# Kernel optimization log

Hardware: AMD Instinct MI355X
Metric: run time of the kernel (lower is better)

## Reference

```python
import jax, jax.numpy as jnp
import numpy as np

NUM_HEADS = 12


def setup_inputs() -> dict:
    key = jax.random.key(0)
    k1, k2, k3, k4 = jax.random.split(key, 4)
    dim = 768
    B, N1, N2 = 8, 64, 4096  # N1 must equal head_dim = dim // num_heads
    x = jax.random.normal(k1, (B, N1, dim), dtype=jnp.float32)
    y = jax.random.normal(k2, (B, N2, dim), dtype=jnp.float32)
    # torch nn.Linear layout: [out_features, in_features]
    W_qkv = jax.random.normal(k3, (3 * dim, dim), dtype=jnp.float32) * 0.02
    W_proj = jax.random.normal(k4, (dim, dim), dtype=jnp.float32) * 0.02
    b_proj = jnp.zeros((dim,), dtype=jnp.float32)
    return {"x": x, "y": y, "W_qkv": W_qkv, "W_proj": W_proj, "b_proj": b_proj}


def _split_heads(t, H):
    # [B, N, C] -> [B, H, N, C//H]
    B, N, C = t.shape
    return t.reshape(B, N, H, C // H).transpose(0, 2, 1, 3)


def reference(x, y, W_qkv, W_proj, b_proj):
    H = NUM_HEADS
    B1, N1, C = x.shape
    B2, N2, _ = y.shape
    hd = C // H
    scale = hd ** -0.5

    # qkv projections (bias=False); take q from x, k/v from y
    qkv_x = x @ W_qkv.T                      # [B, N1, 3C]
    q = _split_heads(qkv_x[..., :C], H)      # [B, H, N1, hd]
    qkv_y = y @ W_qkv.T                      # [B, N2, 3C]
    k = _split_heads(qkv_y[..., C:2 * C], H)  # [B, H, N2, hd]
    v = _split_heads(qkv_y[..., 2 * C:], H)   # [B, H, N2, hd]

    attn = jnp.einsum('bhqd,bhkd->bhqk', q, k) * scale  # [B, H, N1, N2]
    attn = jax.nn.softmax(attn, axis=-1)
    attn_t = attn.transpose(0, 1, 3, 2)       # [B, H, N2, N1]; N1 == hd

    # non-standard elementwise combine with v (requires N1 == hd)
    out = attn_t * v                          # [B, H, N2, hd]
    out = out.transpose(0, 2, 1, 3).reshape(B2, N2, C)
    return out @ W_proj.T + b_proj
```

## Files before the change

kernel.cpp:

```cpp
#include <hip/hip_runtime.h>
#include <math.h>


typedef __attribute__((ext_vector_type(8))) short short8;
typedef __attribute__((ext_vector_type(4))) float f32x4;

__device__ __forceinline__ ushort f2bf(float x) {
  unsigned u = __float_as_uint(x);
  u += 0x7fffu + ((u >> 16) & 1u);
  return (ushort)(u >> 16);
}
__device__ __forceinline__ float bf2f(ushort h) {
  return __uint_as_float((unsigned)h << 16);
}

__device__ __forceinline__ void gl_lds16(const ushort* g, ushort* l) {
  __builtin_amdgcn_global_load_lds(
      (__attribute__((address_space(1))) void*)g,
      (__attribute__((address_space(3))) void*)l, 16, 0, 0);
}

__global__ __launch_bounds__(256) void cast_all(
    const float* __restrict__ x, ushort* __restrict__ xb,
    const float* __restrict__ w1, ushort* __restrict__ w1b,
    const float* __restrict__ w2, ushort* __restrict__ w2b,
    const float* __restrict__ y, ushort* __restrict__ yb) {
  long i = (long)(blockIdx.x * 256 + threadIdx.x) * 8;
  if (i >= 27918336L) return;
  const float* s; ushort* d; long off;
  if (i < 393216L)        { s = x;  d = xb;  off = i; }
  else if (i < 2162688L)  { s = w1; d = w1b; off = i - 393216L; }
  else if (i < 2752512L)  { s = w2; d = w2b; off = i - 2162688L; }
  else                    { s = y;  d = yb;  off = i - 2752512L; }
  float4 a = *(const float4*)(s + off);
  float4 b = *(const float4*)(s + off + 4);
  ushort o[8] = {f2bf(a.x), f2bf(a.y), f2bf(a.z), f2bf(a.w),
                 f2bf(b.x), f2bf(b.y), f2bf(b.z), f2bf(b.w)};
  *(uint4*)(d + off) = *(const uint4*)o;
}

template <typename CT>
__device__ __forceinline__ void gemm_body(
    const ushort* __restrict__ A, int lda,
    const ushort* __restrict__ B, int ldb,
    CT* __restrict__ C, int ldc, int K,
    const float* __restrict__ bias, int rt, int ct)
{
  __shared__ __align__(16) ushort As[2][8192];
  __shared__ __align__(16) ushort Bs[2][4096];
  const int tid = threadIdx.x;
  const int m0 = rt * 256, n0 = ct * 128;

  const int w = tid >> 6, lane = tid & 63;
  const int lm = lane & 15, quad = lane >> 4;
  const int WR = (w >> 1) * 128, WC = (w & 1) * 64;

  const ushort* Ag[4];
#pragma unroll
  for (int q = 0; q < 4; ++q) {
    const int G = q * 256 + w * 64 + lane;
    const int row = G >> 2, g = ((G & 3) - (row >> 1)) & 3;
    Ag[q] = A + (size_t)(m0 + row) * lda + g * 8;
  }
  const ushort* Bg[2];
#pragma unroll
  for (int q = 0; q < 2; ++q) {
    const int G = q * 256 + w * 64 + lane;
    const int row = G >> 2, g = ((G & 3) - (row >> 1)) & 3;
    Bg[q] = B + (size_t)(n0 + row) * ldb + g * 8;
  }

  f32x4 acc[8][4];
#pragma unroll
  for (int i = 0; i < 8; ++i)
#pragma unroll
    for (int j = 0; j < 4; ++j) acc[i][j] = (f32x4)(0.f);

  const int nk = K >> 5;
#pragma unroll
  for (int q = 0; q < 4; ++q) gl_lds16(Ag[q], &As[0][q * 2048 + w * 512]);
#pragma unroll
  for (int q = 0; q < 2; ++q) gl_lds16(Bg[q], &Bs[0][q * 2048 + w * 512]);

  int cur = 0;
  for (int kk = 0; kk < nk; ++kk) {
    __syncthreads();
    if (kk + 1 < nk) {
      const int k0 = (kk + 1) << 5;
#pragma unroll
      for (int q = 0; q < 4; ++q) gl_lds16(Ag[q] + k0, &As[cur ^ 1][q * 2048 + w * 512]);
#pragma unroll
      for (int q = 0; q < 2; ++q) gl_lds16(Bg[q] + k0, &Bs[cur ^ 1][q * 2048 + w * 512]);
    }
    const ushort* Ab = &As[cur][0];
    const ushort* Bb = &Bs[cur][0];
    short8 af[8], bf8[4];
#pragma unroll
    for (int i = 0; i < 8; ++i) {
      const int Ra = WR + i * 16 + lm;
      af[i] = *(const short8*)(const void*)(Ab + Ra * 32 + ((quad + (Ra >> 1)) & 3) * 8);
    }
#pragma unroll
    for (int j = 0; j < 4; ++j) {
      const int Rb = WC + j * 16 + lm;
      bf8[j] = *(const short8*)(const void*)(Bb + Rb * 32 + ((quad + (Rb >> 1)) & 3) * 8);
    }
#pragma unroll
    for (int i = 0; i < 8; ++i)
#pragma unroll
      for (int j = 0; j < 4; ++j)
        acc[i][j] = __builtin_amdgcn_mfma_f32_16x16x32_bf16(af[i], bf8[j], acc[i][j], 0, 0, 0);
    cur ^= 1;
  }
  __syncthreads();

  if constexpr (sizeof(CT) == 2) {
    ushort* eb = ((ushort*)&As[0][0]) + w * 2048;
#pragma unroll
    for (int i = 0; i < 8; ++i) {
      ushort* ebc = eb + (i & 1) * 1024;
#pragma unroll
      for (int j = 0; j < 4; ++j)
#pragma unroll
        for (int r = 0; r < 4; ++r) {
          const int R = quad * 4 + r;
          const int gt = j * 2 + (lm >> 3);
          const int gs = (gt + R) & 7;
          ebc[R * 64 + gs * 8 + (lm & 7)] = f2bf(acc[i][j][r]);
        }
#pragma unroll
      for (int p = 0; p < 2; ++p) {
        const int R2 = (lane >> 3) + p * 8;
        const int g = lane & 7;
        const int gt2 = (g - R2) & 7;
        uint4 v = *(const uint4*)(const void*)(ebc + R2 * 64 + g * 8);
        *(uint4*)(C + (size_t)(m0 + WR + i * 16 + R2) * ldc + n0 + WC + gt2 * 8) = v;
      }
    }
  } else {
#pragma unroll
    for (int j = 0; j < 4; ++j) {
      const int col = n0 + WC + j * 16 + lm;
      const float bb = bias ? bias[col] : 0.f;
#pragma unroll
      for (int i = 0; i < 8; ++i) {
        const int row = m0 + WR + i * 16 + quad * 4;
#pragma unroll
        for (int r = 0; r < 4; ++r)
          C[(size_t)(row + r) * ldc + col] = (CT)(acc[i][j][r] + bb);
      }
    }
  }
}

__global__ __launch_bounds__(256, 2) void qkv_gemm(
    const ushort* __restrict__ xbf, const ushort* __restrict__ ybf,
    const ushort* __restrict__ wqkv, ushort* __restrict__ qbf,
    ushort* __restrict__ kvbf)
{
  const int id = blockIdx.x;
  if (id < 1536) {
    const int xcd = id & 7, local = id >> 3;
    const int rt = xcd * 16 + (local & 15);
    const int ct = local >> 4;
    gemm_body<ushort>(ybf, 768, wqkv + (size_t)768 * 768, 768, kvbf, 1536, 768,
                      nullptr, rt, ct);
  } else {
    const int q = id - 1536;
    gemm_body<ushort>(xbf, 768, wqkv, 768, qbf, 768, 768, nullptr, q & 1, q >> 1);
  }
}

__global__ __launch_bounds__(256, 2) void out_gemm(
    const ushort* __restrict__ Ebf, const ushort* __restrict__ wpbf,
    const float* __restrict__ bias, float* __restrict__ out)
{
  const int id = blockIdx.x;
  const int xcd = id & 7, local = id >> 3;
  const int rt = xcd * 16 + (local & 15);
  const int ct = local >> 4;
  gemm_body<float>(Ebf, 768, wpbf, 768, out, 768, 768, bias, rt, ct);
}

__global__ __launch_bounds__(256) void attn_pass1(
    const ushort* __restrict__ Q,
    const ushort* __restrict__ KV,
    float* __restrict__ parts)
{
  const int chunk = blockIdx.x, h = blockIdx.y, b = blockIdx.z;
  const int tid = threadIdx.x;
  __shared__ __align__(16) ushort Qs[64 * 72];
  __shared__ __align__(16) ushort Ks[128 * 72];
  __shared__ float sm[4][64], ss[4][64];
#pragma unroll
  for (int p = 0; p < 2; ++p) {
    const int G = tid + 256 * p, row = G >> 3, g = G & 7;
    *(uint4*)(Qs + row * 72 + g * 8) =
        *(const uint4*)(Q + (size_t)(b * 64 + row) * 768 + h * 64 + g * 8);
  }
#pragma unroll
  for (int p = 0; p < 4; ++p) {
    const int G = tid + 256 * p, row = G >> 3, g = G & 7;
    *(uint4*)(Ks + row * 72 + g * 8) =
        *(const uint4*)(KV + (size_t)(b * 4096 + chunk * 128 + row) * 1536 + h * 64 + g * 8);
  }
  __syncthreads();

  const int w = tid >> 6, lane = tid & 63;
  const int lm = lane & 15, quad = lane >> 4;
  const int wn = w * 32;

  f32x4 acc[4][2];
#pragma unroll
  for (int i = 0; i < 4; ++i) { acc[i][0] = (f32x4)(0.f); acc[i][1] = (f32x4)(0.f); }
#pragma unroll
  for (int s = 0; s < 2; ++s) {
    short8 qf[4], kf[2];
#pragma unroll
    for (int i = 0; i < 4; ++i)
      qf[i] = *(const short8*)(const void*)(Qs + (i * 16 + lm) * 72 + s * 32 + quad * 8);
#pragma unroll
    for (int jn = 0; jn < 2; ++jn)
      kf[jn] = *(const short8*)(const void*)(Ks + (wn + jn * 16 + lm) * 72 + s * 32 + quad * 8);
#pragma unroll
    for (int i = 0; i < 4; ++i)
#pragma unroll
      for (int jn = 0; jn < 2; ++jn)
        acc[i][jn] = __builtin_amdgcn_mfma_f32_16x16x32_bf16(qf[i], kf[jn], acc[i][jn], 0, 0, 0);
  }

#pragma unroll
  for (int i = 0; i < 4; ++i)
#pragma unroll
    for (int r = 0; r < 4; ++r) {
      float v0 = acc[i][0][r] * 0.125f, v1 = acc[i][1][r] * 0.125f;
      float m = fmaxf(v0, v1);
      m = fmaxf(m, __shfl_xor(m, 1)); m = fmaxf(m, __shfl_xor(m, 2));
      m = fmaxf(m, __shfl_xor(m, 4)); m = fmaxf(m, __shfl_xor(m, 8));
      float e = __expf(v0 - m) + __expf(v1 - m);
      e += __shfl_xor(e, 1); e += __shfl_xor(e, 2);
      e += __shfl_xor(e, 4); e += __shfl_xor(e, 8);
      if (lm == 0) {
        const int j = i * 16 + quad * 4 + r;
        sm[w][j] = m; ss[w][j] = e;
      }
    }
  __syncthreads();
  if (tid < 64) {
    float g = fmaxf(fmaxf(sm[0][tid], sm[1][tid]), fmaxf(sm[2][tid], sm[3][tid]));
    float s = ss[0][tid] * __expf(sm[0][tid] - g) + ss[1][tid] * __expf(sm[1][tid] - g)
            + ss[2][tid] * __expf(sm[2][tid] - g) + ss[3][tid] * __expf(sm[3][tid] - g);
    const int bh = b * 12 + h;
    float* p = parts + ((size_t)(bh * 32 + chunk) * 64 + tid) * 2;
    p[0] = g; p[1] = s;
  }
}

__global__ __launch_bounds__(256) void attn_pass2(
    const ushort* __restrict__ Q, const ushort* __restrict__ KV,
    const float* __restrict__ parts, ushort* __restrict__ E)
{
  const int chunk = blockIdx.x, h = blockIdx.y, b = blockIdx.z;
  const int tid = threadIdx.x;
  __shared__ __align__(16) ushort Qs[64 * 72];
  __shared__ __align__(16) ushort Ks[128 * 72];
  __shared__ __align__(16) ushort Vs[128 * 72];
  __shared__ float st[64][2];
#pragma unroll
  for (int p = 0; p < 2; ++p) {
    const int G = tid + 256 * p, row = G >> 3, g = G & 7;
    *(uint4*)(Qs + row * 72 + g * 8) =
        *(const uint4*)(Q + (size_t)(b * 64 + row) * 768 + h * 64 + g * 8);
  }
#pragma unroll
  for (int p = 0; p < 4; ++p) {
    const int G = tid + 256 * p, row = G >> 3, g = G & 7;
    const size_t rbase = (size_t)(b * 4096 + chunk * 128 + row) * 1536 + h * 64 + g * 8;
    *(uint4*)(Ks + row * 72 + g * 8) = *(const uint4*)(KV + rbase);
    *(uint4*)(Vs + row * 72 + g * 8) = *(const uint4*)(KV + rbase + 768);
  }
  {
    const int bh = b * 12 + h;
    const int tq = tid >> 2, tc = tid & 3;
    float pm[8], ps[8];
    float gm = -1e30f;
#pragma unroll
    for (int c = 0; c < 8; ++c) {
      const float* p = parts + ((size_t)(bh * 32 + tc * 8 + c) * 64 + tq) * 2;
      pm[c] = p[0]; ps[c] = p[1];
      gm = fmaxf(gm, pm[c]);
    }
    gm = fmaxf(gm, __shfl_xor(gm, 1));
    gm = fmaxf(gm, __shfl_xor(gm, 2));
    float s = 0.f;
#pragma unroll
    for (int c = 0; c < 8; ++c) s += ps[c] * __expf(pm[c] - gm);
    s += __shfl_xor(s, 1);
    s += __shfl_xor(s, 2);
    if (tc == 0) { st[tq][0] = gm; st[tq][1] = 1.f / s; }
  }
  __syncthreads();

  const int w = tid >> 6, lane = tid & 63;
  const int lm = lane & 15, quad = lane >> 4;
  const int wn = w * 32;

  f32x4 acc[4][2];
#pragma unroll
  for (int i = 0; i < 4; ++i) { acc[i][0] = (f32x4)(0.f); acc[i][1] = (f32x4)(0.f); }
#pragma unroll
  for (int s = 0; s < 2; ++s) {
    short8 qf[4], kf[2];
#pragma unroll
    for (int i = 0; i < 4; ++i)
      qf[i] = *(const short8*)(const void*)(Qs + (i * 16 + lm) * 72 + s * 32 + quad * 8);
#pragma unroll
    for (int jn = 0; jn < 2; ++jn)
      kf[jn] = *(const short8*)(const void*)(Ks + (wn + jn * 16 + lm) * 72 + s * 32 + quad * 8);
#pragma unroll
    for (int i = 0; i < 4; ++i)
#pragma unroll
      for (int jn = 0; jn < 2; ++jn)
        acc[i][jn] = __builtin_amdgcn_mfma_f32_16x16x32_bf16(qf[i], kf[jn], acc[i][jn], 0, 0, 0);
  }

  ushort ev[4][2][4];
#pragma unroll
  for (int i = 0; i < 4; ++i)
#pragma unroll
    for (int jn = 0; jn < 2; ++jn)
#pragma unroll
      for (int r = 0; r < 4; ++r) {
        const float v = acc[i][jn][r] * 0.125f;
        const int j = i * 16 + quad * 4 + r;
        const float p = __expf(v - st[j][0]) * st[j][1];
        const int key = wn + jn * 16 + lm;
        ev[i][jn][r] = f2bf(p * bf2f(Vs[key * 72 + j]));
      }
  __syncthreads();
  ushort* Es = Ks;
#pragma unroll
  for (int i = 0; i < 4; ++i)
#pragma unroll
    for (int jn = 0; jn < 2; ++jn)
#pragma unroll
      for (int r = 0; r < 4; ++r)
        Es[(wn + jn * 16 + lm) * 72 + i * 16 + quad * 4 + r] = ev[i][jn][r];
  __syncthreads();
#pragma unroll
  for (int k = 0; k < 4; ++k) {
    const int row = tid >> 1, g = (tid & 1) * 4 + k;
    uint4 v = *(const uint4*)(const void*)(Es + row * 72 + g * 8);
    *(uint4*)(E + (size_t)(b * 4096 + chunk * 128 + row) * 768 + h * 64 + g * 8) = v;
  }
}

extern "C" void kernel_launch(void* const* d_in, const int* in_sizes, int n_in,
                              void* d_out, int out_size, void* d_ws, size_t ws_size,
                              hipStream_t stream) {
  const float* x     = (const float*)d_in[0];
  const float* y     = (const float*)d_in[1];
  const float* Wqkv  = (const float*)d_in[2];
  const float* Wproj = (const float*)d_in[3];
  const float* bproj = (const float*)d_in[4];
  float* out = (float*)d_out;

  char* wsb = (char*)d_ws;
  ushort* xbf    = (ushort*)(wsb + 0);
  ushort* qbf    = (ushort*)(wsb + 786432);
  ushort* wqkvbf = (ushort*)(wsb + 1572864);
  float*  parts  = (float*)(wsb + 1572864);
  ushort* wpbf   = (ushort*)(wsb + 5111808);
  ushort* ybf    = (ushort*)(wsb + 6291456);
  ushort* Ebf    = ybf;
  ushort* KVbf   = (ushort*)(wsb + 56623104);

  cast_all<<<13632, 256, 0, stream>>>(x, xbf, Wqkv, wqkvbf, Wproj, wpbf, y, ybf);

  qkv_gemm<<<1548, 256, 0, stream>>>(xbf, ybf, wqkvbf, qbf, KVbf);

  attn_pass1<<<dim3(32, 12, 8), 256, 0, stream>>>(qbf, KVbf, parts);
  attn_pass2<<<dim3(32, 12, 8), 256, 0, stream>>>(qbf, KVbf, parts, Ebf);

  out_gemm<<<768, 256, 0, stream>>>(Ebf, wpbf, bproj, out);
}
```

Before: 427.3 us.

## Use 8-wave 256x256 pipelined GEMM for KV and output projections

Replaces the 4-wave 256x128 GEMM body with an 8-wave 256x256 tile. It uses a K-step of 64, XOR-swizzled LDS, staggered global-to-LDS prefetch of A and B interleaved with MFMA phases, and s_setprio around the MFMA blocks. The small Q projection is split into its own 128x128-tile kernel instead of sharing the combined launch. The larger tile is meant to raise arithmetic intensity and overlap loads with compute. In exchange it uses 128KB of LDS per block, which limits occupancy to one block per CU, and its manual waitcnt and barrier scheduling is fragile.

```diff
diff --git a/kernel.cpp b/kernel.cpp
--- a/kernel.cpp
+++ b/kernel.cpp
@@ -40,34 +40,30 @@
 }
 
 template <typename CT>
-__device__ __forceinline__ void gemm_body(
+__device__ __forceinline__ void gemm8_body(
     const ushort* __restrict__ A, int lda,
     const ushort* __restrict__ B, int ldb,
-    CT* __restrict__ C, int ldc, int K,
+    CT* __restrict__ C, int ldc,
     const float* __restrict__ bias, int rt, int ct)
 {
-  __shared__ __align__(16) ushort As[2][8192];
-  __shared__ __align__(16) ushort Bs[2][4096];
+  constexpr int NK = 12;
+  __shared__ __align__(16) ushort Abuf[2][16384];
+  __shared__ __align__(16) ushort Bbuf[2][16384];
   const int tid = threadIdx.x;
-  const int m0 = rt * 256, n0 = ct * 128;
-
-  const int w = tid >> 6, lane = tid & 63;
+  const int m0 = rt * 256, n0 = ct * 256;
+  const int wv = tid >> 6, lane = tid & 63;
   const int lm = lane & 15, quad = lane >> 4;
-  const int WR = (w >> 1) * 128, WC = (w & 1) * 64;
-
+  const int WR = (wv >> 2) * 128, WC = (wv & 3) * 64;
+
+  const int srow = lane >> 3;
+  const int sg = (lane & 7) ^ srow;
   const ushort* Ag[4];
-#pragma unroll
-  for (int q = 0; q < 4; ++q) {
-    const int G = q * 256 + w * 64 + lane;
-    const int row = G >> 2, g = ((G & 3) - (row >> 1)) & 3;
-    Ag[q] = A + (size_t)(m0 + row) * lda + g * 8;
-  }
-  const ushort* Bg[2];
-#pragma unroll
-  for (int q = 0; q < 2; ++q) {
-    const int G = q * 256 + w * 64 + lane;
-    const int row = G >> 2, g = ((G & 3) - (row >> 1)) & 3;
-    Bg[q] = B + (size_t)(n0 + row) * ldb + g * 8;
+  const ushort* Bg[4];
+#pragma unroll
+  for (int j = 0; j < 4; ++j) {
+    const int r = (wv * 4 + j) * 8 + srow;
+    Ag[j] = A + (size_t)(m0 + r) * lda + sg * 8;
+    Bg[j] = B + (size_t)(n0 + r) * ldb + sg * 8;
   }
 
   f32x4 acc[8][4];
@@ -76,46 +72,72 @@
 #pragma unroll
     for (int j = 0; j < 4; ++j) acc[i][j] = (f32x4)(0.f);
 
-  const int nk = K >> 5;
-#pragma unroll
-  for (int q = 0; q < 4; ++q) gl_lds16(Ag[q], &As[0][q * 2048 + w * 512]);
-#pragma unroll
-  for (int q = 0; q < 2; ++q) gl_lds16(Bg[q], &Bs[0][q * 2048 + w * 512]);
-
-  int cur = 0;
-  for (int kk = 0; kk < nk; ++kk) {
-    __syncthreads();
-    if (kk + 1 < nk) {
-      const int k0 = (kk + 1) << 5;
-#pragma unroll
-      for (int q = 0; q < 4; ++q) gl_lds16(Ag[q] + k0, &As[cur ^ 1][q * 2048 + w * 512]);
-#pragma unroll
-      for (int q = 0; q < 2; ++q) gl_lds16(Bg[q] + k0, &Bs[cur ^ 1][q * 2048 + w * 512]);
-    }
-    const ushort* Ab = &As[cur][0];
-    const ushort* Bb = &Bs[cur][0];
-    short8 af[8], bf8[4];
-#pragma unroll
-    for (int i = 0; i < 8; ++i) {
-      const int Ra = WR + i * 16 + lm;
-      af[i] = *(const short8*)(const void*)(Ab + Ra * 32 + ((quad + (Ra >> 1)) & 3) * 8);
-    }
-#pragma unroll
-    for (int j = 0; j < 4; ++j) {
-      const int Rb = WC + j * 16 + lm;
-      bf8[j] = *(const short8*)(const void*)(Bb + Rb * 32 + ((quad + (Rb >> 1)) & 3) * 8);
-    }
-#pragma unroll
-    for (int i = 0; i < 8; ++i)
-#pragma unroll
-      for (int j = 0; j < 4; ++j)
-        acc[i][j] = __builtin_amdgcn_mfma_f32_16x16x32_bf16(af[i], bf8[j], acc[i][j], 0, 0, 0);
-    cur ^= 1;
+#pragma unroll
+  for (int j = 0; j < 4; ++j) gl_lds16(Ag[j], &Abuf[0][(wv * 4 + j) * 512]);
+#pragma unroll
+  for (int j = 0; j < 4; ++j) gl_lds16(Bg[j], &Bbuf[0][(wv * 4 + j) * 512]);
+#pragma unroll
+  for (int j = 0; j < 4; ++j) gl_lds16(Bg[j] + 64, &Bbuf[1][(wv * 4 + j) * 512]);
+  asm volatile("s_waitcnt vmcnt(4)" ::: "memory");
+  __builtin_amdgcn_s_barrier();
+
+#pragma unroll 1
+  for (int T = 0; T < NK; ++T) {
+    const ushort* Ab = &Abuf[T & 1][0];
+    const ushort* Bb = &Bbuf[T & 1][0];
+    ushort* An = &Abuf[(T & 1) ^ 1][0];
+    ushort* Bn = &Bbuf[T & 1][0];
+    const int k1 = (T + 1) * 64, k2 = (T + 2) * 64;
+    const bool stA = (T + 1 < NK), stB = (T + 2 < NK);
+    short8 bfr[4][2];
+
+#pragma unroll
+    for (int q = 0; q < 4; ++q) {
+      if (q == 0) {
+#pragma unroll
+        for (int n = 0; n < 4; ++n)
+#pragma unroll
+          for (int ks = 0; ks < 2; ++ks)
+            bfr[n][ks] = *(const short8*)(const void*)(
+                Bb + (WC + n * 16 + lm) * 64 + ((ks * 4 + quad) ^ (lm & 7)) * 8);
+      }
+      short8 af[2][2];
+#pragma unroll
+      for (int i = 0; i < 2; ++i)
+#pragma unroll
+        for (int ks = 0; ks < 2; ++ks)
+          af[i][ks] = *(const short8*)(const void*)(
+              Ab + (WR + (q * 2 + i) * 16 + lm) * 64 + ((ks * 4 + quad) ^ (lm & 7)) * 8);
+      if (q == 0 && stA) { gl_lds16(Ag[0] + k1, An + (wv * 4 + 0) * 512);
+                           gl_lds16(Ag[1] + k1, An + (wv * 4 + 1) * 512); }
+      if (q == 1 && stA) { gl_lds16(Ag[2] + k1, An + (wv * 4 + 2) * 512);
+                           gl_lds16(Ag[3] + k1, An + (wv * 4 + 3) * 512); }
+      if (q == 2 && stB) { gl_lds16(Bg[0] + k2, Bn + (wv * 4 + 0) * 512);
+                           gl_lds16(Bg[1] + k2, Bn + (wv * 4 + 1) * 512); }
+      if (q == 3 && stB) { gl_lds16(Bg[2] + k2, Bn + (wv * 4 + 2) * 512);
+                           gl_lds16(Bg[3] + k2, Bn + (wv * 4 + 3) * 512); }
+      __builtin_amdgcn_s_barrier();
+      __builtin_amdgcn_s_setprio(1);
+#pragma unroll
+      for (int i = 0; i < 2; ++i)
+#pragma unroll
+        for (int n = 0; n < 4; ++n)
+#pragma unroll
+          for (int ks = 0; ks < 2; ++ks)
+            acc[q * 2 + i][n] = __builtin_amdgcn_mfma_f32_16x16x32_bf16(
+                af[i][ks], bfr[n][ks], acc[q * 2 + i][n], 0, 0, 0);
+      __builtin_amdgcn_s_setprio(0);
+      if (q == 3) {
+        if (stB) asm volatile("s_waitcnt vmcnt(4)" ::: "memory");
+        else     asm volatile("s_waitcnt vmcnt(0)" ::: "memory");
+      }
+      __builtin_amdgcn_s_barrier();
+    }
   }
   __syncthreads();
 
   if constexpr (sizeof(CT) == 2) {
-    ushort* eb = ((ushort*)&As[0][0]) + w * 2048;
+    ushort* eb = ((ushort*)&Abuf[0][0]) + wv * 2048;
 #pragma unroll
     for (int i = 0; i < 8; ++i) {
       ushort* ebc = eb + (i & 1) * 1024;
@@ -153,33 +175,111 @@
   }
 }
 
-__global__ __launch_bounds__(256, 2) void qkv_gemm(
-    const ushort* __restrict__ xbf, const ushort* __restrict__ ybf,
-    const ushort* __restrict__ wqkv, ushort* __restrict__ qbf,
+__global__ __launch_bounds__(512, 2) void kv_gemm8(
+    const ushort* __restrict__ ybf, const ushort* __restrict__ wkv,
     ushort* __restrict__ kvbf)
-{
-  const int id = blockIdx.x;
-  if (id < 1536) {
-    const int xcd = id & 7, local = id >> 3;
-    const int rt = xcd * 16 + (local & 15);
-    const int ct = local >> 4;
-    gemm_body<ushort>(ybf, 768, wqkv + (size_t)768 * 768, 768, kvbf, 1536, 768,
-                      nullptr, rt, ct);
-  } else {
-    const int q = id - 1536;
-    gemm_body<ushort>(xbf, 768, wqkv, 768, qbf, 768, 768, nullptr, q & 1, q >> 1);
-  }
-}
-
-__global__ __launch_bounds__(256, 2) void out_gemm(
-    const ushort* __restrict__ Ebf, const ushort* __restrict__ wpbf,
-    const float* __restrict__ bias, float* __restrict__ out)
 {
   const int id = blockIdx.x;
   const int xcd = id & 7, local = id >> 3;
   const int rt = xcd * 16 + (local & 15);
   const int ct = local >> 4;
-  gemm_body<float>(Ebf, 768, wpbf, 768, out, 768, 768, bias, rt, ct);
+  gemm8_body<ushort>(ybf, 768, wkv, 768, kvbf, 1536, nullptr, rt, ct);
+}
+
+__global__ __launch_bounds__(512, 2) void out_gemm8(
+    const ushort* __restrict__ Ebf, const ushort* __restrict__ wpbf,
+    const float* __restrict__ bias, float* __restrict__ out)
+{
+  const int id = blockIdx.x;
+  const int xcd = id & 7, local = id >> 3;
+  const int rt = xcd * 16 + (local & 15);
+  const int ct = local >> 4;
+  gemm8_body<float>(Ebf, 768, wpbf, 768, out, 768, bias, rt, ct);
+}
+
+__global__ __launch_bounds__(256) void q_gemm(
+    const ushort* __restrict__ A, const ushort* __restrict__ B,
+    ushort* __restrict__ C)
+{
+  constexpr int lda = 768, ldb = 768, ldc = 768, K = 768;
+  __shared__ __align__(16) ushort As[2][4096];
+  __shared__ __align__(16) ushort Bs[2][4096];
+  const int tid = threadIdx.x;
+  const int rt = blockIdx.x & 3, ct = blockIdx.x >> 2;
+  const int m0 = rt * 128, n0 = ct * 128;
+
+  const int w = tid >> 6, lane = tid & 63;
+  const int lm = lane & 15, quad = lane >> 4;
+  const int wm = (w & 1) * 64, wn = (w >> 1) * 64;
+
+  const int G0 = w * 64 + lane, G1 = G0 + 256;
+  const int r0 = G0 >> 2, c0 = ((G0 & 3) - (r0 >> 1)) & 3;
+  const int r1 = G1 >> 2, c1 = ((G1 & 3) - (r1 >> 1)) & 3;
+  const ushort* Ag0 = A + (size_t)(m0 + r0) * lda + c0 * 8;
+  const ushort* Ag1 = A + (size_t)(m0 + r1) * lda + c1 * 8;
+  const ushort* Bg0 = B + (size_t)(n0 + r0) * ldb + c0 * 8;
+  const ushort* Bg1 = B + (size_t)(n0 + r1) * ldb + c1 * 8;
+  const int lds0 = w * 512, lds1 = w * 512 + 2048;
+
+  f32x4 acc[4][4];
+#pragma unroll
+  for (int i = 0; i < 4; ++i)
+#pragma unroll
+    for (int j = 0; j < 4; ++j) acc[i][j] = (f32x4)(0.f);
+
+  const int nk = K >> 5;
+  gl_lds16(Ag0, &As[0][lds0]); gl_lds16(Ag1, &As[0][lds1]);
+  gl_lds16(Bg0, &Bs[0][lds0]); gl_lds16(Bg1, &Bs[0][lds1]);
+
+  int cur = 0;
+  for (int kk = 0; kk < nk; ++kk) {
+    __syncthreads();
+    if (kk + 1 < nk) {
+      const int k0 = (kk + 1) << 5;
+      gl_lds16(Ag0 + k0, &As[cur ^ 1][lds0]); gl_lds16(Ag1 + k0, &As[cur ^ 1][lds1]);
+      gl_lds16(Bg0 + k0, &Bs[cur ^ 1][lds0]); gl_lds16(Bg1 + k0, &Bs[cur ^ 1][lds1]);
+    }
+    const ushort* Ab = &As[cur][0];
+    const ushort* Bb = &Bs[cur][0];
+    short8 af[4], bf8[4];
+#pragma unroll
+    for (int i = 0; i < 4; ++i) {
+      const int Ra = wm + i * 16 + lm;
+      af[i] = *(const short8*)(const void*)(Ab + Ra * 32 + ((quad + (Ra >> 1)) & 3) * 8);
+      const int Rb = wn + i * 16 + lm;
+      bf8[i] = *(const short8*)(const void*)(Bb + Rb * 32 + ((quad + (Rb >> 1)) & 3) * 8);
+    }
+#pragma unroll
+    for (int i = 0; i < 4; ++i)
+#pragma unroll
+      for (int j = 0; j < 4; ++j)
+        acc[i][j] = __builtin_amdgcn_mfma_f32_16x16x32_bf16(af[i], bf8[j], acc[i][j], 0, 0, 0);
+    cur ^= 1;
+  }
+  __syncthreads();
+
+  ushort* eb = ((ushort*)&Bs[0][0]) + w * 2048;
+#pragma unroll
+  for (int i = 0; i < 4; ++i) {
+    ushort* ebc = eb + (i & 1) * 1024;
+#pragma unroll
+    for (int j = 0; j < 4; ++j)
+#pragma unroll
+      for (int r = 0; r < 4; ++r) {
+        const int R = quad * 4 + r;
+        const int gt = j * 2 + (lm >> 3);
+        const int gs = (gt + R) & 7;
+        ebc[R * 64 + gs * 8 + (lm & 7)] = f2bf(acc[i][j][r]);
+      }
+#pragma unroll
+    for (int p = 0; p < 2; ++p) {
+      const int R2 = (lane >> 3) + p * 8;
+      const int g = lane & 7;
+      const int gt2 = (g - R2) & 7;
+      uint4 v = *(const uint4*)(const void*)(ebc + R2 * 64 + g * 8);
+      *(uint4*)(C + (size_t)(m0 + wm + i * 16 + R2) * ldc + n0 + wn + gt2 * 8) = v;
+    }
+  }
 }
 
 __global__ __launch_bounds__(256) void attn_pass1(
@@ -377,10 +477,12 @@
 
   cast_all<<<13632, 256, 0, stream>>>(x, xbf, Wqkv, wqkvbf, Wproj, wpbf, y, ybf);
 
-  qkv_gemm<<<1548, 256, 0, stream>>>(xbf, ybf, wqkvbf, qbf, KVbf);
+  q_gemm<<<24, 256, 0, stream>>>(xbf, wqkvbf, qbf);
+
+  kv_gemm8<<<768, 512, 0, stream>>>(ybf, wqkvbf + (size_t)768 * 768, KVbf);
 
   attn_pass1<<<dim3(32, 12, 8), 256, 0, stream>>>(qbf, KVbf, parts);
   attn_pass2<<<dim3(32, 12, 8), 256, 0, stream>>>(qbf, KVbf, parts, Ebf);
 
-  out_gemm<<<768, 256, 0, stream>>>(Ebf, wpbf, bproj, out);
-}
+  out_gemm8<<<384, 512, 0, stream>>>(Ebf, wpbf, bproj, out);
+}
```

After: 413.3 us. -3.3%, faster.
